# Performance work log

Measured on AMD Instinct MI355X. Metric: run time of the kernel, lower is better.

## Reference

```python
import jax, jax.numpy as jnp
import numpy as np

D_MODEL = 1024
FFN = 4096
N_EXPERTS = 8
TOPK = 2
B, L = 4, 2048


def setup_inputs() -> dict:
    key = jax.random.key(0)
    ks = jax.random.split(key, 8)
    s_in = 1.0 / np.sqrt(D_MODEL)
    s_ffn = 1.0 / np.sqrt(FFN)
    x = jax.random.normal(ks[0], (B, L, D_MODEL), dtype=jnp.float32)
    gate_w = jax.random.uniform(ks[1], (D_MODEL, N_EXPERTS), jnp.float32, -s_in, s_in)
    gate_b = jax.random.uniform(ks[2], (N_EXPERTS,), jnp.float32, -s_in, s_in)
    w1 = jax.random.uniform(ks[3], (N_EXPERTS, D_MODEL, FFN), jnp.float32, -s_in, s_in)
    b1 = jax.random.uniform(ks[4], (N_EXPERTS, FFN), jnp.float32, -s_in, s_in)
    w2 = jax.random.uniform(ks[5], (N_EXPERTS, FFN, D_MODEL), jnp.float32, -s_ffn, s_ffn)
    b2 = jax.random.uniform(ks[6], (N_EXPERTS, D_MODEL), jnp.float32, -s_ffn, s_ffn)
    return {"x": x, "gate_w": gate_w, "gate_b": gate_b,
            "w1": w1, "b1": b1, "w2": w2, "b2": b2}


def _moe(x, gate_w, gate_b, w1, b1, w2, b2):
    bs, l, d = x.shape
    T = bs * l
    xf = x.reshape(T, d)                       # [T, D]
    # --- TopkRouter: sparse softmax over top-k gate logits ---
    logits = xf @ gate_w + gate_b              # [T, E]
    top_vals, top_idx = jax.lax.top_k(logits, TOPK)
    rows = jnp.arange(T)[:, None]
    sparse = jnp.full_like(logits, -jnp.inf).at[rows, top_idx].set(top_vals)
    gates = jax.nn.softmax(sparse, axis=-1)    # [T, E], zero for non-topk experts
    # --- per-expert FFN, combined with gate weights (gate==0 => no contribution,
    # identical math to the original masked gather/scatter loop, eval mode) ---
    out = jnp.zeros_like(xf)
    for e in range(N_EXPERTS):
        h = jax.nn.gelu(xf @ w1[e] + b1[e], approximate=False)  # exact GELU (torch default)
        y = h @ w2[e] + b2[e]
        out = out + gates[:, e:e + 1] * y
    return out.reshape(bs, l, d)


def reference(x, gate_w, gate_b, w1, b1, w2, b2):
    return _moe(x, gate_w, gate_b, w1, b1, w2, b2)
```

## Files before the change

### kernel.cpp

```cpp
#include <hip/hip_runtime.h>
#include <hip/hip_bf16.h>
#include <math.h>
#include <stdint.h>

#define T_TOKENS 8192
#define DM 1024
#define FFNDIM 4096
#define NE 8
#define CAP 8192
#define SMAX 18432

typedef __attribute__((ext_vector_type(8))) __bf16 bf16x8;
typedef __attribute__((ext_vector_type(4))) __bf16 bf16x4;
typedef __attribute__((ext_vector_type(4))) float f32x4;

__device__ __forceinline__ float gelu_exact(float v) {
    return 0.5f * v * (1.0f + erff(v * 0.70710678118654752440f));
}

union PK8 { __bf16 h[8]; uint4 v; };

__device__ __forceinline__ void gload16(const void* g, void* l) {
    __builtin_amdgcn_global_load_lds(
        (const __attribute__((address_space(1))) uint32_t*)g,
        (__attribute__((address_space(3))) uint32_t*)l, 16, 0, 0);
}

__device__ __forceinline__ int xcd_swz(int nwg) {
    int orig = blockIdx.x;
    int xcd = orig & 7, loc = orig >> 3;
    int q = nwg >> 3, r = nwg & 7;
    int base = (xcd < r) ? xcd * (q + 1) : r * (q + 1) + (xcd - r) * q;
    return base + loc;
}

__global__ void zero_counts_kernel(int* __restrict__ counts) {
    if (threadIdx.x < NE) counts[threadIdx.x] = 0;
}

__global__ __launch_bounds__(256) void zero_out_kernel(float* __restrict__ out,
                                                       int* __restrict__ counts) {
    size_t i = (size_t)blockIdx.x * 256 + threadIdx.x;
    uint4 z = make_uint4(0u, 0u, 0u, 0u);
    uint4* p = (uint4*)out + i * 2;
    p[0] = z; p[1] = z;
    if (blockIdx.x == 0 && threadIdx.x < NE) counts[threadIdx.x] = 0;
}

__global__ __launch_bounds__(256) void cvt_x_kernel(const float* __restrict__ x,
                                                    __bf16* __restrict__ xb) {
    size_t i = ((size_t)blockIdx.x * 256 + threadIdx.x) * 8;
    f32x4 a = *(const f32x4*)(x + i);
    f32x4 b = *(const f32x4*)(x + i + 4);
    PK8 u;
#pragma unroll
    for (int j = 0; j < 4; ++j) { u.h[j] = (__bf16)a[j]; u.h[4 + j] = (__bf16)b[j]; }
    *(uint4*)(xb + i) = u.v;
}

__global__ __launch_bounds__(256) void transpose_cvt_kernel(
        const float* __restrict__ w, __bf16* __restrict__ wt, int K, int N) {
    __shared__ __bf16 tile[64][72];
    int ntb = blockIdx.x, ktb = blockIdx.y, e = blockIdx.z;
    const float* src = w + ((size_t)e * K + (size_t)ktb * 64) * N + ntb * 64;
    int t = threadIdx.x;
    int tx = t & 15, ty = t >> 4;
#pragma unroll
    for (int rr = 0; rr < 4; ++rr) {
        int r = ty + rr * 16;
        f32x4 v = *(const f32x4*)(src + (size_t)r * N + tx * 4);
#pragma unroll
        for (int j = 0; j < 4; ++j) tile[tx * 4 + j][r] = (__bf16)v[j];
    }
    __syncthreads();
    int ow = t & 7, oy = t >> 3;
#pragma unroll
    for (int rr = 0; rr < 2; ++rr) {
        int n = oy + rr * 32;
        uint4 val = *(const uint4*)&tile[n][ow * 8];
        *(uint4*)(wt + ((size_t)e * N + (size_t)ntb * 64 + n) * K
                  + (size_t)ktb * 64 + ow * 8) = val;
    }
}

__global__ __launch_bounds__(256) void router_kernel(
        const float* __restrict__ x, const float* __restrict__ gate_w,
        const float* __restrict__ gate_b, int* __restrict__ counts,
        int* __restrict__ idx_list, float* __restrict__ gate_list,
        uint32_t* __restrict__ pack) {
    int wave = threadIdx.x >> 6, lane = threadIdx.x & 63;
    int tk = blockIdx.x * 4 + wave;
    const float* xr = x + (size_t)tk * DM;
    float acc[NE];
#pragma unroll
    for (int e = 0; e < NE; ++e) acc[e] = 0.f;
#pragma unroll
    for (int i = 0; i < DM / 64; ++i) {
        int d = i * 64 + lane;
        float xv = xr[d];
        f32x4 g0v = *(const f32x4*)(gate_w + d * NE);
        f32x4 g1v = *(const f32x4*)(gate_w + d * NE + 4);
#pragma unroll
        for (int e = 0; e < 4; ++e) { acc[e] += xv * g0v[e]; acc[4 + e] += xv * g1v[e]; }
    }
#pragma unroll
    for (int e = 0; e < NE; ++e) {
#pragma unroll
        for (int m = 32; m > 0; m >>= 1) acc[e] += __shfl_xor(acc[e], m, 64);
    }
    if (lane == 0) {
        float v0 = -INFINITY, v1 = -INFINITY;
        int i0 = 0, i1 = 0;
#pragma unroll
        for (int e = 0; e < NE; ++e) {
            float l = acc[e] + gate_b[e];
            if (l > v0) { v1 = v0; i1 = i0; v0 = l; i0 = e; }
            else if (l > v1) { v1 = l; i1 = e; }
        }
        float g0 = 1.f / (1.f + expf(v1 - v0));
        float g1 = 1.f - g0;
        int p0 = atomicAdd(&counts[i0], 1);
        idx_list[i0 * CAP + p0] = tk;
        gate_list[i0 * CAP + p0] = g0;
        int p1 = atomicAdd(&counts[i1], 1);
        idx_list[i1 * CAP + p1] = tk;
        gate_list[i1 * CAP + p1] = g1;
        pack[tk] = ((uint32_t)((i0 << 13) | p0) << 16) | (uint32_t)((i1 << 13) | p1);
    }
}

__global__ void scan_kernel(const int* __restrict__ counts, int* __restrict__ pbase) {
    if (threadIdx.x == 0 && blockIdx.x == 0) {
        int s = 0;
        for (int e = 0; e < NE; ++e) { pbase[e] = s; s += (counts[e] + 255) & ~255; }
        pbase[NE] = s;
    }
}

__device__ __forceinline__ int find_expert(const int* pbase, int slot_tile) {
    int e = 0;
#pragma unroll
    for (int k = 0; k < NE - 1; ++k)
        if (pbase[k + 1] <= slot_tile) e = k + 1;
    return e;
}


__global__ __launch_bounds__(512, 2) void gemm1_kernel(
        const __bf16* __restrict__ xb, const __bf16* __restrict__ w1t,
        const float* __restrict__ b1, const int* __restrict__ counts,
        const int* __restrict__ pbase, const int* __restrict__ idx_list,
        __bf16* __restrict__ h, int chunk_start) {
    __shared__ __bf16 Al[2][256 * 32];
    __shared__ __bf16 Bl[2][256 * 32];

    int wid = xcd_swz(gridDim.x);
    int mtl = wid >> 4, nt = wid & 15;

    int slot_tile = chunk_start + mtl * 256;
    if (slot_tile >= pbase[NE]) return;
    int e = find_expert(pbase, slot_tile);
    int cnt = counts[e];
    int loc = slot_tile - pbase[e];
    if (loc >= cnt) return;

    int t = threadIdx.x, lane = t & 63, wave = t >> 6;

    const char* asrc[2];
    const char* bsrc[2];
    uint32_t dofs[2];
#pragma unroll
    for (int q = 0; q < 2; ++q) {
        int row = (wave * 2 + q) * 16 + (lane >> 2);
        int ch  = lane & 3;
        int sw  = ((ch ^ ((row >> 1) & 3)) << 4);
        int lc = loc + row; if (lc > cnt - 1) lc = cnt - 1;
        int tok = idx_list[e * CAP + lc];
        asrc[q] = (const char*)(xb + (size_t)tok * DM) + sw;
        bsrc[q] = (const char*)(w1t + ((size_t)e * FFNDIM + nt * 256 + row) * DM) + sw;
        dofs[q] = (uint32_t)(wave * 2 + q) * 1024;
    }

    int wr = wave >> 2, wc = wave & 3;
    int l15 = lane & 15, quad = lane >> 4;

    f32x4 acc[8][4];
#pragma unroll
    for (int i = 0; i < 8; ++i)
#pragma unroll
        for (int j = 0; j < 4; ++j) acc[i][j] = f32x4{0.f, 0.f, 0.f, 0.f};

#pragma unroll
    for (int q = 0; q < 2; ++q) {
        gload16(asrc[q], (char*)Al[0] + dofs[q]);
        gload16(bsrc[q], (char*)Bl[0] + dofs[q]);
    }
    __syncthreads();

    const int NSTEP = DM / 32;
    for (int st = 0; st < NSTEP; ++st) {
        int cur = st & 1;
        if (st + 1 < NSTEP) {
            int off = (st + 1) * 64;
#pragma unroll
            for (int q = 0; q < 2; ++q) {
                gload16(asrc[q] + off, (char*)Al[cur ^ 1] + dofs[q]);
                gload16(bsrc[q] + off, (char*)Bl[cur ^ 1] + dofs[q]);
            }
        }
        const __bf16* A = Al[cur];
        const __bf16* B = Bl[cur];
        bf16x8 af[8], bfr[4];
#pragma unroll
        for (int i = 0; i < 8; ++i) {
            int m = wr * 128 + i * 16 + l15;
            af[i] = *(const bf16x8*)(A + m * 32 + ((quad ^ ((m >> 1) & 3)) << 3));
        }
#pragma unroll
        for (int j = 0; j < 4; ++j) {
            int n = wc * 64 + j * 16 + l15;
            bfr[j] = *(const bf16x8*)(B + n * 32 + ((quad ^ ((n >> 1) & 3)) << 3));
        }
#pragma unroll
        for (int i = 0; i < 8; ++i)
#pragma unroll
            for (int j = 0; j < 4; ++j)
                acc[i][j] = __builtin_amdgcn_mfma_f32_16x16x32_bf16(
                    af[i], bfr[j], acc[i][j], 0, 0, 0);
        __syncthreads();
    }

    float bias[4];
#pragma unroll
    for (int j = 0; j < 4; ++j)
        bias[j] = b1[(size_t)e * FFNDIM + nt * 256 + wc * 64 + j * 16 + l15];
#pragma unroll
    for (int i = 0; i < 8; ++i) {
#pragma unroll
        for (int r = 0; r < 4; ++r) {
            int rowl = wr * 128 + i * 16 + quad * 4 + r;
            if (loc + rowl < cnt) {
                size_t hoff = (size_t)(mtl * 256 + rowl) * FFNDIM + nt * 256;
#pragma unroll
                for (int j = 0; j < 4; ++j) {
                    float v = acc[i][j][r] + bias[j];
                    h[hoff + wc * 64 + j * 16 + l15] = (__bf16)gelu_exact(v);
                }
            }
        }
    }
}

template<int YM>
__global__ __launch_bounds__(512, 2) void gemm2_kernel(
        const __bf16* __restrict__ h, const __bf16* __restrict__ w2t,
        const float* __restrict__ b2, const int* __restrict__ counts,
        const int* __restrict__ pbase, const int* __restrict__ idx_list,
        const float* __restrict__ gate_list, float* __restrict__ out,
        void* __restrict__ ybuf, int chunk_start) {
    __shared__ __bf16 Al[2][256 * 32];
    __shared__ __bf16 Bl[2][256 * 32];

    int wid = xcd_swz(gridDim.x);
    int mtl = wid >> 2, nt = wid & 3;

    int slot_tile = chunk_start + mtl * 256;
    if (slot_tile >= pbase[NE]) return;
    int e = find_expert(pbase, slot_tile);
    int cnt = counts[e];
    int loc = slot_tile - pbase[e];
    if (loc >= cnt) return;

    int t = threadIdx.x, lane = t & 63, wave = t >> 6;

    const char* asrc[2];
    const char* bsrc[2];
    uint32_t dofs[2];
#pragma unroll
    for (int q = 0; q < 2; ++q) {
        int row = (wave * 2 + q) * 16 + (lane >> 2);
        int ch  = lane & 3;
        int sw  = ((ch ^ ((row >> 1) & 3)) << 4);
        asrc[q] = (const char*)(h + (size_t)(mtl * 256 + row) * FFNDIM) + sw;
        bsrc[q] = (const char*)(w2t + ((size_t)e * DM + nt * 256 + row) * FFNDIM) + sw;
        dofs[q] = (uint32_t)(wave * 2 + q) * 1024;
    }

    int wr = wave >> 2, wc = wave & 3;
    int l15 = lane & 15, quad = lane >> 4;

    f32x4 acc[8][4];
#pragma unroll
    for (int i = 0; i < 8; ++i)
#pragma unroll
        for (int j = 0; j < 4; ++j) acc[i][j] = f32x4{0.f, 0.f, 0.f, 0.f};

#pragma unroll
    for (int q = 0; q < 2; ++q) {
        gload16(asrc[q], (char*)Al[0] + dofs[q]);
        gload16(bsrc[q], (char*)Bl[0] + dofs[q]);
    }
    __syncthreads();

    const int NSTEP = FFNDIM / 32;
    for (int st = 0; st < NSTEP; ++st) {
        int cur = st & 1;
        if (st + 1 < NSTEP) {
            int off = (st + 1) * 64;
#pragma unroll
            for (int q = 0; q < 2; ++q) {
                gload16(asrc[q] + off, (char*)Al[cur ^ 1] + dofs[q]);
                gload16(bsrc[q] + off, (char*)Bl[cur ^ 1] + dofs[q]);
            }
        }
        const __bf16* A = Al[cur];
        const __bf16* B = Bl[cur];
        bf16x8 af[8], bfr[4];
#pragma unroll
        for (int i = 0; i < 8; ++i) {
            int m = wr * 128 + i * 16 + l15;
            af[i] = *(const bf16x8*)(A + m * 32 + ((quad ^ ((m >> 1) & 3)) << 3));
        }
#pragma unroll
        for (int j = 0; j < 4; ++j) {
            int n = wc * 64 + j * 16 + l15;
            bfr[j] = *(const bf16x8*)(B + n * 32 + ((quad ^ ((n >> 1) & 3)) << 3));
        }
#pragma unroll
        for (int i = 0; i < 8; ++i)
#pragma unroll
            for (int j = 0; j < 4; ++j)
                acc[i][j] = __builtin_amdgcn_mfma_f32_16x16x32_bf16(
                    af[i], bfr[j], acc[i][j], 0, 0, 0);
        __syncthreads();
    }

    float b2v[4];
#pragma unroll
    for (int j = 0; j < 4; ++j)
        b2v[j] = b2[(size_t)e * DM + nt * 256 + wc * 64 + j * 16 + l15];
#pragma unroll
    for (int i = 0; i < 8; ++i) {
#pragma unroll
        for (int r = 0; r < 4; ++r) {
            int rowl = wr * 128 + i * 16 + quad * 4 + r;
            int local = loc + rowl;
            if (local < cnt) {
                float g = gate_list[e * CAP + local];
                if (YM == 0) {
                    int tok = idx_list[e * CAP + local];
                    float* orow = out + (size_t)tok * DM + nt * 256;
#pragma unroll
                    for (int j = 0; j < 4; ++j)
                        atomicAdd(orow + wc * 64 + j * 16 + l15,
                                  g * (acc[i][j][r] + b2v[j]));
                } else {
                    size_t yoff = (size_t)(slot_tile + rowl) * DM + nt * 256;
                    if (YM == 1) {
                        float* yr = (float*)ybuf + yoff;
#pragma unroll
                        for (int j = 0; j < 4; ++j)
                            yr[wc * 64 + j * 16 + l15] = g * (acc[i][j][r] + b2v[j]);
                    } else {
                        __bf16* yr = (__bf16*)ybuf + yoff;
#pragma unroll
                        for (int j = 0; j < 4; ++j)
                            yr[wc * 64 + j * 16 + l15] =
                                (__bf16)(g * (acc[i][j][r] + b2v[j]));
                    }
                }
            }
        }
    }
}

template<int YM>
__global__ __launch_bounds__(256) void combine_kernel(
        const void* __restrict__ ybuf, const uint32_t* __restrict__ pack,
        const int* __restrict__ pbase, float* __restrict__ out) {
    int tk = blockIdx.x;
    uint32_t pk = pack[tk];
    uint32_t a = pk >> 16, b = pk & 0xffffu;
    size_t sa = (size_t)pbase[a >> 13] + (a & 8191u);
    size_t sb = (size_t)pbase[b >> 13] + (b & 8191u);
    int d = threadIdx.x * 4;
    f32x4 vo;
    if (YM == 1) {
        const float* y = (const float*)ybuf;
        f32x4 va = *(const f32x4*)(y + sa * DM + d);
        f32x4 vb = *(const f32x4*)(y + sb * DM + d);
#pragma unroll
        for (int j = 0; j < 4; ++j) vo[j] = va[j] + vb[j];
    } else {
        const __bf16* y = (const __bf16*)ybuf;
        bf16x4 va = *(const bf16x4*)(y + sa * DM + d);
        bf16x4 vb = *(const bf16x4*)(y + sb * DM + d);
#pragma unroll
        for (int j = 0; j < 4; ++j) vo[j] = (float)va[j] + (float)vb[j];
    }
    *(f32x4*)(out + (size_t)tk * DM + d) = vo;
}

extern "C" void kernel_launch(void* const* d_in, const int* in_sizes, int n_in,
                              void* d_out, int out_size, void* d_ws, size_t ws_size,
                              hipStream_t stream) {
    const float* x      = (const float*)d_in[0];
    const float* gate_w = (const float*)d_in[1];
    const float* gate_b = (const float*)d_in[2];
    const float* w1     = (const float*)d_in[3];
    const float* b1     = (const float*)d_in[4];
    const float* w2     = (const float*)d_in[5];
    const float* b2     = (const float*)d_in[6];
    float* out = (float*)d_out;

    char* wsb = (char*)d_ws;
    int*      counts   = (int*)wsb;
    int*      pbase    = (int*)(wsb + 64);
    int*      idx_list = (int*)(wsb + 128);
    float*    gate_lst = (float*)(wsb + 128 + 262144);
    uint32_t* pack     = (uint32_t*)(wsb + 128 + 524288);
    const size_t FIXED = 557184;
    const size_t W_ELEMS = (size_t)NE * DM * FFNDIM;
    __bf16* w1t = (__bf16*)(wsb + FIXED);
    __bf16* w2t = w1t + W_ELEMS;
    __bf16* xb  = w2t + W_ELEMS;
    char*   dyn = (char*)(xb + (size_t)T_TOKENS * DM);
    const size_t DYNBASE = FIXED + 4 * W_ELEMS + (size_t)T_TOKENS * DM * 2;
    size_t avail = ws_size > DYNBASE ? ws_size - DYNBASE : 0;

    const size_t YB32 = (size_t)SMAX * DM * 4;
    const size_t YB16 = (size_t)SMAX * DM * 2;
    int S, NCH, YM;
    if      (avail >= YB32 + 18432ull * 8192) { S = 18432; NCH = 1; YM = 1; }
    else if (avail >= YB32 + 9216ull * 8192)  { S = 9216;  NCH = 2; YM = 1; }
    else if (avail >= YB16 + 9216ull * 8192)  { S = 9216;  NCH = 2; YM = 2; }
    else if (avail >= YB16 + 4608ull * 8192)  { S = 4608;  NCH = 4; YM = 2; }
    else                                      { S = 2304;  NCH = 8; YM = 0; }
    char*   ybuf = dyn;
    __bf16* hbuf = (__bf16*)(dyn + (YM == 1 ? YB32 : YM == 2 ? YB16 : 0));

    cvt_x_kernel<<<4096, 256, 0, stream>>>(x, xb);
    transpose_cvt_kernel<<<dim3(FFNDIM / 64, DM / 64, NE), 256, 0, stream>>>(
        w1, w1t, DM, FFNDIM);
    transpose_cvt_kernel<<<dim3(DM / 64, FFNDIM / 64, NE), 256, 0, stream>>>(
        w2, w2t, FFNDIM, DM);
    if (YM) zero_counts_kernel<<<1, 64, 0, stream>>>(counts);
    else    zero_out_kernel<<<4096, 256, 0, stream>>>(out, counts);
    router_kernel<<<2048, 256, 0, stream>>>(x, gate_w, gate_b, counts, idx_list,
                                            gate_lst, pack);
    scan_kernel<<<1, 64, 0, stream>>>(counts, pbase);

    int MT = S / 256;
    for (int c = 0; c < NCH; ++c) {
        gemm1_kernel<<<dim3(MT * 16), 512, 0, stream>>>(xb, w1t, b1, counts, pbase,
                                                        idx_list, hbuf, c * S);
        if (YM == 1)
            gemm2_kernel<1><<<dim3(MT * 4), 512, 0, stream>>>(
                hbuf, w2t, b2, counts, pbase, idx_list, gate_lst, out, ybuf, c * S);
        else if (YM == 2)
            gemm2_kernel<2><<<dim3(MT * 4), 512, 0, stream>>>(
                hbuf, w2t, b2, counts, pbase, idx_list, gate_lst, out, ybuf, c * S);
        else
            gemm2_kernel<0><<<dim3(MT * 4), 512, 0, stream>>>(
                hbuf, w2t, b2, counts, pbase, idx_list, gate_lst, out, ybuf, c * S);
    }
    if (YM == 1)
        combine_kernel<1><<<dim3(T_TOKENS), 256, 0, stream>>>(ybuf, pack, pbase, out);
    else if (YM == 2)
        combine_kernel<2><<<dim3(T_TOKENS), 256, 0, stream>>>(ybuf, pack, pbase, out);
}
```

Baseline: 1.265 ms.

## Use 4-stage LDS ring pipeline in expert GEMMs and fuse x conversion into router

Result: faster. 1.156 ms (-8.6%).

```diff
diff --git a/kernel.cpp b/kernel.cpp
--- a/kernel.cpp
+++ b/kernel.cpp
@@ -47,17 +47,6 @@
     if (blockIdx.x == 0 && threadIdx.x < NE) counts[threadIdx.x] = 0;
 }
 
-__global__ __launch_bounds__(256) void cvt_x_kernel(const float* __restrict__ x,
-                                                    __bf16* __restrict__ xb) {
-    size_t i = ((size_t)blockIdx.x * 256 + threadIdx.x) * 8;
-    f32x4 a = *(const f32x4*)(x + i);
-    f32x4 b = *(const f32x4*)(x + i + 4);
-    PK8 u;
-#pragma unroll
-    for (int j = 0; j < 4; ++j) { u.h[j] = (__bf16)a[j]; u.h[4 + j] = (__bf16)b[j]; }
-    *(uint4*)(xb + i) = u.v;
-}
-
 __global__ __launch_bounds__(256) void transpose_cvt_kernel(
         const float* __restrict__ w, __bf16* __restrict__ wt, int K, int N) {
     __shared__ __bf16 tile[64][72];
@@ -87,7 +76,7 @@
         const float* __restrict__ x, const float* __restrict__ gate_w,
         const float* __restrict__ gate_b, int* __restrict__ counts,
         int* __restrict__ idx_list, float* __restrict__ gate_list,
-        uint32_t* __restrict__ pack) {
+        uint32_t* __restrict__ pack, __bf16* __restrict__ xb) {
     int wave = threadIdx.x >> 6, lane = threadIdx.x & 63;
     int tk = blockIdx.x * 4 + wave;
     const float* xr = x + (size_t)tk * DM;
@@ -98,6 +87,7 @@
     for (int i = 0; i < DM / 64; ++i) {
         int d = i * 64 + lane;
         float xv = xr[d];
+        xb[(size_t)tk * DM + d] = (__bf16)xv;
         f32x4 g0v = *(const f32x4*)(gate_w + d * NE);
         f32x4 g1v = *(const f32x4*)(gate_w + d * NE + 4);
 #pragma unroll
@@ -146,13 +136,18 @@
 }
 
 
+#define RING_WAIT(rem_)                                              \
+    if ((rem_) >= 2)      asm volatile("s_waitcnt vmcnt(8)" ::: "memory"); \
+    else if ((rem_) == 1) asm volatile("s_waitcnt vmcnt(4)" ::: "memory"); \
+    else                  asm volatile("s_waitcnt vmcnt(0)" ::: "memory");
+
 __global__ __launch_bounds__(512, 2) void gemm1_kernel(
         const __bf16* __restrict__ xb, const __bf16* __restrict__ w1t,
         const float* __restrict__ b1, const int* __restrict__ counts,
         const int* __restrict__ pbase, const int* __restrict__ idx_list,
         __bf16* __restrict__ h, int chunk_start) {
-    __shared__ __bf16 Al[2][256 * 32];
-    __shared__ __bf16 Bl[2][256 * 32];
+    __shared__ __bf16 Al[4][256 * 32];
+    __shared__ __bf16 Bl[4][256 * 32];
 
     int wid = xcd_swz(gridDim.x);
     int mtl = wid >> 4, nt = wid & 15;
@@ -191,25 +186,29 @@
         for (int j = 0; j < 4; ++j) acc[i][j] = f32x4{0.f, 0.f, 0.f, 0.f};
 
 #pragma unroll
-    for (int q = 0; q < 2; ++q) {
-        gload16(asrc[q], (char*)Al[0] + dofs[q]);
-        gload16(bsrc[q], (char*)Bl[0] + dofs[q]);
-    }
-    __syncthreads();
+    for (int s = 0; s < 3; ++s)
+#pragma unroll
+        for (int q = 0; q < 2; ++q) {
+            gload16(asrc[q] + s * 64, (char*)Al[s] + dofs[q]);
+            gload16(bsrc[q] + s * 64, (char*)Bl[s] + dofs[q]);
+        }
 
     const int NSTEP = DM / 32;
+#pragma unroll 1
     for (int st = 0; st < NSTEP; ++st) {
-        int cur = st & 1;
-        if (st + 1 < NSTEP) {
-            int off = (st + 1) * 64;
+        int rem = NSTEP - 1 - st;
+        RING_WAIT(rem);
+        __builtin_amdgcn_s_barrier();
+        if (st + 3 < NSTEP) {
+            int s = st + 3, b = s & 3, off = s * 64;
 #pragma unroll
             for (int q = 0; q < 2; ++q) {
-                gload16(asrc[q] + off, (char*)Al[cur ^ 1] + dofs[q]);
-                gload16(bsrc[q] + off, (char*)Bl[cur ^ 1] + dofs[q]);
+                gload16(asrc[q] + off, (char*)Al[b] + dofs[q]);
+                gload16(bsrc[q] + off, (char*)Bl[b] + dofs[q]);
             }
         }
-        const __bf16* A = Al[cur];
-        const __bf16* B = Bl[cur];
+        const __bf16* A = Al[st & 3];
+        const __bf16* B = Bl[st & 3];
         bf16x8 af[8], bfr[4];
 #pragma unroll
         for (int i = 0; i < 8; ++i) {
@@ -221,13 +220,14 @@
             int n = wc * 64 + j * 16 + l15;
             bfr[j] = *(const bf16x8*)(B + n * 32 + ((quad ^ ((n >> 1) & 3)) << 3));
         }
+        __builtin_amdgcn_s_setprio(1);
 #pragma unroll
         for (int i = 0; i < 8; ++i)
 #pragma unroll
             for (int j = 0; j < 4; ++j)
                 acc[i][j] = __builtin_amdgcn_mfma_f32_16x16x32_bf16(
                     af[i], bfr[j], acc[i][j], 0, 0, 0);
-        __syncthreads();
+        __builtin_amdgcn_s_setprio(0);
     }
 
     float bias[4];
@@ -258,8 +258,8 @@
         const int* __restrict__ pbase, const int* __restrict__ idx_list,
         const float* __restrict__ gate_list, float* __restrict__ out,
         void* __restrict__ ybuf, int chunk_start) {
-    __shared__ __bf16 Al[2][256 * 32];
-    __shared__ __bf16 Bl[2][256 * 32];
+    __shared__ __bf16 Al[4][256 * 32];
+    __shared__ __bf16 Bl[4][256 * 32];
 
     int wid = xcd_swz(gridDim.x);
     int mtl = wid >> 2, nt = wid & 3;
@@ -296,25 +296,29 @@
         for (int j = 0; j < 4; ++j) acc[i][j] = f32x4{0.f, 0.f, 0.f, 0.f};
 
 #pragma unroll
-    for (int q = 0; q < 2; ++q) {
-        gload16(asrc[q], (char*)Al[0] + dofs[q]);
-        gload16(bsrc[q], (char*)Bl[0] + dofs[q]);
-    }
-    __syncthreads();
+    for (int s = 0; s < 3; ++s)
+#pragma unroll
+        for (int q = 0; q < 2; ++q) {
+            gload16(asrc[q] + s * 64, (char*)Al[s] + dofs[q]);
+            gload16(bsrc[q] + s * 64, (char*)Bl[s] + dofs[q]);
+        }
 
     const int NSTEP = FFNDIM / 32;
+#pragma unroll 1
     for (int st = 0; st < NSTEP; ++st) {
-        int cur = st & 1;
-        if (st + 1 < NSTEP) {
-            int off = (st + 1) * 64;
+        int rem = NSTEP - 1 - st;
+        RING_WAIT(rem);
+        __builtin_amdgcn_s_barrier();
+        if (st + 3 < NSTEP) {
+            int s = st + 3, b = s & 3, off = s * 64;
 #pragma unroll
             for (int q = 0; q < 2; ++q) {
-                gload16(asrc[q] + off, (char*)Al[cur ^ 1] + dofs[q]);
-                gload16(bsrc[q] + off, (char*)Bl[cur ^ 1] + dofs[q]);
+                gload16(asrc[q] + off, (char*)Al[b] + dofs[q]);
+                gload16(bsrc[q] + off, (char*)Bl[b] + dofs[q]);
             }
         }
-        const __bf16* A = Al[cur];
-        const __bf16* B = Bl[cur];
+        const __bf16* A = Al[st & 3];
+        const __bf16* B = Bl[st & 3];
         bf16x8 af[8], bfr[4];
 #pragma unroll
         for (int i = 0; i < 8; ++i) {
@@ -326,13 +330,14 @@
             int n = wc * 64 + j * 16 + l15;
             bfr[j] = *(const bf16x8*)(B + n * 32 + ((quad ^ ((n >> 1) & 3)) << 3));
         }
+        __builtin_amdgcn_s_setprio(1);
 #pragma unroll
         for (int i = 0; i < 8; ++i)
 #pragma unroll
             for (int j = 0; j < 4; ++j)
                 acc[i][j] = __builtin_amdgcn_mfma_f32_16x16x32_bf16(
                     af[i], bfr[j], acc[i][j], 0, 0, 0);
-        __syncthreads();
+        __builtin_amdgcn_s_setprio(0);
     }
 
     float b2v[4];
@@ -439,7 +444,6 @@
     char*   ybuf = dyn;
     __bf16* hbuf = (__bf16*)(dyn + (YM == 1 ? YB32 : YM == 2 ? YB16 : 0));
 
-    cvt_x_kernel<<<4096, 256, 0, stream>>>(x, xb);
     transpose_cvt_kernel<<<dim3(FFNDIM / 64, DM / 64, NE), 256, 0, stream>>>(
         w1, w1t, DM, FFNDIM);
     transpose_cvt_kernel<<<dim3(DM / 64, FFNDIM / 64, NE), 256, 0, stream>>>(
@@ -447,7 +451,7 @@
     if (YM) zero_counts_kernel<<<1, 64, 0, stream>>>(counts);
     else    zero_out_kernel<<<4096, 256, 0, stream>>>(out, counts);
     router_kernel<<<2048, 256, 0, stream>>>(x, gate_w, gate_b, counts, idx_list,
-                                            gate_lst, pack);
+                                            gate_lst, pack, xb);
     scan_kernel<<<1, 64, 0, stream>>>(counts, pbase);
 
     int MT = S / 256;
```
